# Performance work log

Hardware: AMD Instinct MI355X
Metric: run time of the kernel (lower is better)

Reference implementation:

```python
import jax, jax.numpy as jnp
import numpy as np

DIM = 768
HID = 3072
HID2 = HID // 2
MAX_LEVEL = 8
N_LEV = MAX_LEVEL + 1
BATCH, SEQ = 2, 2048
EPS = 1e-5


def _layernorm(x, gamma, beta):
    m = jnp.mean(x, axis=-1, keepdims=True)
    v = jnp.mean(jnp.square(x - m), axis=-1, keepdims=True)
    return (x - m) * jax.lax.rsqrt(v + EPS) * gamma + beta


def setup_inputs() -> dict:
    key = jax.random.key(0)
    ks = jax.random.split(key, 12)
    s = 0.02
    return {
        "x": jax.random.normal(ks[0], (BATCH, SEQ, DIM), dtype=jnp.float32),
        "levels_info": jax.random.randint(ks[1], (SEQ, 4), 0, N_LEV, dtype=jnp.int32),
        "gamma": jnp.ones((DIM,), dtype=jnp.float32),
        "beta": jnp.zeros((DIM,), dtype=jnp.float32),
        "W1": jax.random.normal(ks[2], (DIM, HID), dtype=jnp.float32) * s,
        "b1": jnp.zeros((HID,), dtype=jnp.float32),
        "W2": jax.random.normal(ks[3], (HID, DIM), dtype=jnp.float32) * s,
        "b2": jnp.zeros((DIM,), dtype=jnp.float32),
        "A1": jax.random.normal(ks[4], (N_LEV, DIM, HID2), dtype=jnp.float32) * s,
        "a1b": jnp.zeros((N_LEV, HID2), dtype=jnp.float32),
        "A2": jax.random.normal(ks[5], (N_LEV, HID2, DIM), dtype=jnp.float32) * s,
        "a2b": jnp.zeros((N_LEV, DIM), dtype=jnp.float32),
        "lmw": jnp.ones((N_LEV,), dtype=jnp.float32)
        + jax.random.normal(ks[6], (N_LEV,), dtype=jnp.float32) * 0.1,
    }


def reference(x, levels_info, gamma, beta, W1, b1, W2, b2, A1, a1b, A2, a2b, lmw):
    # x: [B,S,D]
    x_norm = _layernorm(x, gamma, beta)
    # main MLP: Linear -> GELU (exact, torch default) -> Linear; dropout=0 is identity
    h = jax.nn.gelu(jnp.einsum("bsd,dh->bsh", x_norm, W1) + b1, approximate=False)
    main_out = jnp.einsum("bsh,hd->bsd", h, W2) + b2

    # per-token depth-indexed adapter routing
    depths = jnp.clip(levels_info[:, 0], 0, MAX_LEVEL)  # [S]
    level_adapted = jnp.zeros_like(main_out)
    for lvl in range(N_LEV):  # small fixed expert set
        mask = (depths == lvl).astype(x.dtype)[None, :, None]  # [1,S,1]
        hl = jax.nn.relu(jnp.einsum("bsd,dh->bsh", x_norm, A1[lvl]) + a1b[lvl])
        level_adapted = level_adapted + mask * (
            jnp.einsum("bsh,hd->bsd", hl, A2[lvl]) + a2b[lvl]
        )

    # softmax over the sequence axis (faithful to F.softmax(..., dim=0))
    mix = jax.nn.softmax(lmw[depths], axis=0)[None, :, None]  # [1,S,1]
    return main_out * (1.0 - mix) + level_adapted * mix
```

## Files before the change

kernel.cpp:

```cpp
#include <hip/hip_runtime.h>
#include <hip/hip_bf16.h>
#include <math.h>

typedef __bf16 bf16;
typedef __bf16 bf16x4 __attribute__((ext_vector_type(4)));
typedef __bf16 bf16x8 __attribute__((ext_vector_type(8)));
typedef float f32x4 __attribute__((ext_vector_type(4)));

#define DIM 768
#define HID 3072
#define HID2 1536
#define NLEV 9
#define SEQ 2048
#define ROWS 4096
#define MAXPAD 5248
#define MAXTILES 41

__device__ __forceinline__ void gld16(const void* g, void* l) {
    __builtin_amdgcn_global_load_lds(
        (const __attribute__((address_space(1))) void*)g,
        (__attribute__((address_space(3))) void*)l, 16, 0, 0);
}

__device__ __forceinline__ float fast_gelu(float v) {
    float v2 = v * v;
    float twou = v * (1.59576912f + 0.071354816f * v2);
    float t = __expf(twou);
    return v * t / (t + 1.0f);
}


__device__ __forceinline__ void ln_body(int row, float* sm,
                                        const float* __restrict__ x,
                                        const float* __restrict__ gamma,
                                        const float* __restrict__ beta,
                                        bf16* __restrict__ xn) {
    int tid = threadIdx.x;
    const float* xr = x + (size_t)row * DIM;
    float v0 = xr[tid], v1 = xr[tid + 256], v2 = xr[tid + 512];
    float s = v0 + v1 + v2;
    float q = v0 * v0 + v1 * v1 + v2 * v2;
    for (int off = 32; off; off >>= 1) {
        s += __shfl_down(s, off, 64);
        q += __shfl_down(q, off, 64);
    }
    int wv = tid >> 6, ln = tid & 63;
    if (ln == 0) { sm[wv] = s; sm[4 + wv] = q; }
    __syncthreads();
    if (tid == 0) {
        float S = sm[0] + sm[1] + sm[2] + sm[3];
        float Q = sm[4] + sm[5] + sm[6] + sm[7];
        float m = S * (1.0f / DIM);
        float var = Q * (1.0f / DIM) - m * m;
        sm[8] = m;
        sm[9] = rsqrtf(var + 1e-5f);
    }
    __syncthreads();
    float m = sm[8], r = sm[9];
    bf16* xo = xn + (size_t)row * DIM;
    xo[tid]       = (bf16)((v0 - m) * r * gamma[tid]       + beta[tid]);
    xo[tid + 256] = (bf16)((v1 - m) * r * gamma[tid + 256] + beta[tid + 256]);
    xo[tid + 512] = (bf16)((v2 - m) * r * gamma[tid + 512] + beta[tid + 512]);
}

__device__ __forceinline__ void transpose_body64(float* sm,
                                                 const float* __restrict__ inb,
                                                 bf16* __restrict__ outb,
                                                 int R, int C, int bx, int by) {
    int tid = threadIdx.x;
    int ty = tid >> 4;
    int tx4 = (tid & 15) * 4;
#pragma unroll
    for (int p = 0; p < 4; p++) {
        int rloc = p * 16 + ty;
        int row = by * 64 + rloc;
        float4 v = *(const float4*)(inb + (size_t)row * C + bx * 64 + tx4);
        sm[rloc * 65 + tx4 + 0] = v.x;
        sm[rloc * 65 + tx4 + 1] = v.y;
        sm[rloc * 65 + tx4 + 2] = v.z;
        sm[rloc * 65 + tx4 + 3] = v.w;
    }
    __syncthreads();
    int ch = tid & 7;
    int ocb = tid >> 3;
#pragma unroll
    for (int p = 0; p < 2; p++) {
        int oc = p * 32 + ocb;
        bf16x8 tmp;
#pragma unroll
        for (int k = 0; k < 8; k++) tmp[k] = (bf16)sm[(ch * 8 + k) * 65 + oc];
        *(bf16x8*)(outb + (size_t)(bx * 64 + oc) * R + by * 64 + ch * 8) = tmp;
    }
}

__device__ __forceinline__ void routing_body(float* sm,
                                             const int* __restrict__ levels_info,
                                             const float* __restrict__ lmw,
                                             float* __restrict__ mix,
                                             int* __restrict__ row_index,
                                             int* __restrict__ tile_meta,
                                             float* __restrict__ zbuf) {
    int* cnt = (int*)sm;
    int* cur = cnt + NLEV;
    int* off = cur + NLEV;
    float* mixv = (float*)(off + NLEV);
    int tid = threadIdx.x;
    if (tid < NLEV) { cnt[tid] = 0; cur[tid] = 0; }
    __syncthreads();
    for (int s = tid; s < SEQ; s += 256) {
        int d = levels_info[s * 4];
        d = d < 0 ? 0 : (d > 8 ? 8 : d);
        atomicAdd(&cnt[d], 1);
    }
    for (int i = tid; i < MAXPAD; i += 256) row_index[i] = -1;
    for (int i = tid; i < 512; i += 256) zbuf[i] = 0.0f;
    __syncthreads();
    if (tid == 0) {
        float mx = lmw[0];
        for (int l = 1; l < NLEV; l++) mx = fmaxf(mx, lmw[l]);
        float denom = 0.f;
        for (int l = 0; l < NLEV; l++) denom += (float)cnt[l] * expf(lmw[l] - mx);
        float inv = 1.0f / denom;
        int running = 0, t = 0;
        for (int l = 0; l < NLEV; l++) {
            mixv[l] = expf(lmw[l] - mx) * inv;
            off[l] = running;
            int seg = (2 * cnt[l] + 127) & ~127;
            for (int k = 0; k < seg / 128; k++) tile_meta[t++] = l;
            running += seg;
        }
        for (; t < MAXTILES; t++) tile_meta[t] = -1;
    }
    __syncthreads();
    for (int s = tid; s < SEQ; s += 256) {
        int d = levels_info[s * 4];
        d = d < 0 ? 0 : (d > 8 ? 8 : d);
        int p = atomicAdd(&cur[d], 2);
        row_index[off[d] + p]     = s;
        row_index[off[d] + p + 1] = s + SEQ;
        mix[s] = mixv[d];
    }
}

__global__ __launch_bounds__(256) void prep_kernel(const float* __restrict__ x,
                                                   const int* __restrict__ levels_info,
                                                   const float* __restrict__ gamma,
                                                   const float* __restrict__ beta,
                                                   const float* __restrict__ W1,
                                                   const float* __restrict__ A1,
                                                   const float* __restrict__ lmw,
                                                   bf16* __restrict__ Xn,
                                                   bf16* __restrict__ W1t,
                                                   bf16* __restrict__ A1t,
                                                   float* __restrict__ mix,
                                                   int* __restrict__ row_index,
                                                   int* __restrict__ tile_meta,
                                                   float* __restrict__ zbuf) {
    __shared__ __align__(16) float sm[64 * 65];
    int bid = blockIdx.x;
    if (bid == 0) { routing_body(sm, levels_info, lmw, mix, row_index, tile_meta, zbuf); return; }
    bid -= 1;
    if (bid < ROWS) { ln_body(bid, sm, x, gamma, beta, Xn); return; }
    bid -= ROWS;
    if (bid < 576) {
        transpose_body64(sm, W1, W1t, DIM, HID, bid % 48, bid / 48);
        return;
    }
    bid -= 576;
    {
        int bz = bid / 288, r = bid % 288;
        transpose_body64(sm, A1 + (size_t)bz * DIM * HID2, A1t + (size_t)bz * DIM * HID2,
                         DIM, HID2, r % 24, r / 24);
    }
}

template<int KT>
__device__ __forceinline__ void gemm_loop_db(const bf16* ga0, const bf16* ga1,
                                             const bf16* gb0, const bf16* gb1,
                                             bf16* As, bf16* Bs,
                                             f32x4 (&acc)[4][4]) {
    int tid = threadIdx.x;
    int wv = tid >> 6;
    int lane = tid & 63;
    int wm = wv >> 1, wn = wv & 1;
    int swz = (lane >> 1) & 3;
    int achunk = ((lane >> 4) ^ swz) * 8;
    int aoff = ((wm * 64) + (lane & 15)) * 32 + achunk;
    int boff = ((wn * 64) + (lane & 15)) * 32 + achunk;
    gld16(ga0, As + wv * 512);
    gld16(ga1, As + 2048 + wv * 512);
    gld16(gb0, Bs + wv * 512);
    gld16(gb1, Bs + 2048 + wv * 512);
    ga0 += 32; ga1 += 32; gb0 += 32; gb1 += 32;
#pragma unroll
    for (int kt = 0; kt < KT; ++kt) {
        __syncthreads();
        const int cur = (kt & 1) << 12;
        const int nxt = cur ^ 4096;
        if (kt + 1 < KT) {
            gld16(ga0, As + nxt + wv * 512);
            gld16(ga1, As + nxt + 2048 + wv * 512);
            gld16(gb0, Bs + nxt + wv * 512);
            gld16(gb1, Bs + nxt + 2048 + wv * 512);
            ga0 += 32; ga1 += 32; gb0 += 32; gb1 += 32;
        }
        bf16x8 af[4], bfr[4];
#pragma unroll
        for (int i = 0; i < 4; i++) af[i] = *(const bf16x8*)(As + cur + aoff + i * 512);
#pragma unroll
        for (int j = 0; j < 4; j++) bfr[j] = *(const bf16x8*)(Bs + cur + boff + j * 512);
#pragma unroll
        for (int i = 0; i < 4; i++)
#pragma unroll
            for (int j = 0; j < 4; j++)
                acc[i][j] = __builtin_amdgcn_mfma_f32_16x16x32_bf16(af[i], bfr[j], acc[i][j], 0, 0, 0);
    }
}

#define ACC_INIT(acc) \
    _Pragma("unroll") for (int i = 0; i < 4; i++) \
    _Pragma("unroll") for (int j = 0; j < 4; j++) acc[i][j] = (f32x4){0.f, 0.f, 0.f, 0.f};

#define SWZ_CG(tid) (((tid) & 3) ^ (((tid) >> 3) & 3))

__device__ __forceinline__ void store_tile(const bf16* cbuf, int lane,
                                           bf16* gptr, int ldg) {
#pragma unroll
    for (int p = 0; p < 8; p++) {
        int lrow = p * 8 + (lane >> 3);
        int chunk = (lane & 7) * 8;
        bf16x8 v = *(const bf16x8*)(cbuf + lrow * 64 + chunk);
        *(bf16x8*)(gptr + (size_t)lrow * ldg + chunk) = v;
    }
}

__global__ __launch_bounds__(256) void mlp1_kernel(const bf16* __restrict__ Xn,
                                                   const bf16* __restrict__ W1t,
                                                   const float* __restrict__ b1,
                                                   bf16* __restrict__ H,
                                                   const bf16* __restrict__ A1t,
                                                   const float* __restrict__ a1b,
                                                   const int* __restrict__ row_index,
                                                   const int* __restrict__ tile_meta,
                                                   const bf16* __restrict__ zbuf,
                                                   bf16* __restrict__ HL,
                                                   const float* __restrict__ W2,
                                                   const float* __restrict__ A2,
                                                   bf16* __restrict__ W2t,
                                                   bf16* __restrict__ A2t) {
    __shared__ __align__(16) bf16 smem[16384];
    bf16* As = smem;
    bf16* Bs = smem + 8192;
    int bid = blockIdx.x, tid = threadIdx.x;
    int r0 = tid >> 2, cg = SWZ_CG(tid);
    int lane = tid & 63, wv = tid >> 6, wm = wv >> 1, wn = wv & 1;
    bf16* cbuf = smem + wv * 4096;

    if (bid < 768) {
        int nb = bid / 32, mb = bid % 32;
        f32x4 acc[4][4];
        ACC_INIT(acc);
        const bf16* ga0 = Xn + (size_t)(mb * 128 + r0) * DIM + cg * 8;
        const bf16* ga1 = ga0 + (size_t)64 * DIM;
        const bf16* gb0 = W1t + (size_t)(nb * 128 + r0) * DIM + cg * 8;
        const bf16* gb1 = gb0 + (size_t)64 * DIM;
        gemm_loop_db<24>(ga0, ga1, gb0, gb1, As, Bs, acc);
        int cbase = nb * 128 + wn * 64 + (lane & 15);
        __syncthreads();
#pragma unroll
        for (int j = 0; j < 4; j++) {
            float bias = b1[cbase + j * 16];
#pragma unroll
            for (int i = 0; i < 4; i++)
#pragma unroll
                for (int r = 0; r < 4; r++) {
                    int lrow = i * 16 + ((lane >> 4) << 2) + r;
                    int lcol = j * 16 + (lane & 15);
                    cbuf[lrow * 64 + lcol] = (bf16)fast_gelu(acc[i][j][r] + bias);
                }
        }
        __syncthreads();
        store_tile(cbuf, lane, H + (size_t)(mb * 128 + wm * 64) * HID + nb * 128 + wn * 64, HID);
    } else if (bid < 1260) {
        int t2 = bid - 768;
        int nb = t2 % 12, t = t2 / 12;
        int lvl = tile_meta[t];
        if (lvl < 0) return;
        f32x4 acc[4][4];
        ACC_INIT(acc);
        int ridx0 = row_index[t * 128 + r0];
        int ridx1 = row_index[t * 128 + 64 + r0];
        const bf16* ga0 = (ridx0 >= 0) ? (Xn + (size_t)ridx0 * DIM + cg * 8) : (zbuf + cg * 8);
        const bf16* ga1 = (ridx1 >= 0) ? (Xn + (size_t)ridx1 * DIM + cg * 8) : (zbuf + cg * 8);
        const bf16* Bl = A1t + (size_t)lvl * HID2 * DIM;
        const bf16* gb0 = Bl + (size_t)(nb * 128 + r0) * DIM + cg * 8;
        const bf16* gb1 = gb0 + (size_t)64 * DIM;
        gemm_loop_db<24>(ga0, ga1, gb0, gb1, As, Bs, acc);
        int cbase = nb * 128 + wn * 64 + (lane & 15);
        __syncthreads();
#pragma unroll
        for (int j = 0; j < 4; j++) {
            float bias = a1b[lvl * HID2 + cbase + j * 16];
#pragma unroll
            for (int i = 0; i < 4; i++)
#pragma unroll
                for (int r = 0; r < 4; r++) {
                    int lrow = i * 16 + ((lane >> 4) << 2) + r;
                    int lcol = j * 16 + (lane & 15);
                    cbuf[lrow * 64 + lcol] = (bf16)fmaxf(acc[i][j][r] + bias, 0.0f);
                }
        }
        __syncthreads();
        store_tile(cbuf, lane, HL + (size_t)(t * 128 + wm * 64) * HID2 + nb * 128 + wn * 64, HID2);
    } else if (bid < 1836) {
        int idx = bid - 1260;
        transpose_body64((float*)smem, W2, W2t, HID, DIM, idx % 12, idx / 12);
    } else {
        int idx = bid - 1836;
        int bz = idx / 288, r = idx % 288;
        transpose_body64((float*)smem, A2 + (size_t)bz * HID2 * DIM,
                         A2t + (size_t)bz * HID2 * DIM, HID2, DIM, r % 12, r / 12);
    }
}

__global__ __launch_bounds__(256) void mlp2_kernel(const bf16* __restrict__ H,
                                                   const bf16* __restrict__ W2t,
                                                   bf16* __restrict__ part,
                                                   const bf16* __restrict__ HL,
                                                   const bf16* __restrict__ A2t,
                                                   const float* __restrict__ a2b,
                                                   const int* __restrict__ row_index,
                                                   const int* __restrict__ tile_meta,
                                                   bf16* __restrict__ apart) {
    __shared__ __align__(16) bf16 smem[16384];
    bf16* As = smem;
    bf16* Bs = smem + 8192;
    int bid = blockIdx.x, tid = threadIdx.x;
    int r0 = tid >> 2, cg = SWZ_CG(tid);
    int lane = tid & 63, wv = tid >> 6, wm = wv >> 1, wn = wv & 1;
    bf16* cbuf = smem + wv * 4096;
    f32x4 acc[4][4];
    ACC_INIT(acc);

    if (bid < 384) {
        int cc = bid % 12;
        int nb = cc >> 1, ks = cc & 1;
        int mb = bid / 12;
        const bf16* ga0 = H + (size_t)(mb * 128 + r0) * HID + ks * 1536 + cg * 8;
        const bf16* ga1 = ga0 + (size_t)64 * HID;
        const bf16* gb0 = W2t + (size_t)(nb * 128 + r0) * HID + ks * 1536 + cg * 8;
        const bf16* gb1 = gb0 + (size_t)64 * HID;
        gemm_loop_db<48>(ga0, ga1, gb0, gb1, As, Bs, acc);
        __syncthreads();
#pragma unroll
        for (int j = 0; j < 4; j++)
#pragma unroll
            for (int i = 0; i < 4; i++)
#pragma unroll
                for (int r = 0; r < 4; r++) {
                    int lrow = i * 16 + ((lane >> 4) << 2) + r;
                    int lcol = j * 16 + (lane & 15);
                    cbuf[lrow * 64 + lcol] = (bf16)acc[i][j][r];
                }
        __syncthreads();
        bf16* pk = part + (size_t)ks * ROWS * DIM;
        store_tile(cbuf, lane, pk + (size_t)(mb * 128 + wm * 64) * DIM + nb * 128 + wn * 64, DIM);
    } else {
        int t2 = bid - 384;
        int nb = t2 % 6, t = t2 / 6;
        int lvl = tile_meta[t];
        if (lvl < 0) return;
        const bf16* ga0 = HL + (size_t)(t * 128 + r0) * HID2 + cg * 8;
        const bf16* ga1 = ga0 + (size_t)64 * HID2;
        const bf16* Bl = A2t + (size_t)lvl * DIM * HID2;
        const bf16* gb0 = Bl + (size_t)(nb * 128 + r0) * HID2 + cg * 8;
        const bf16* gb1 = gb0 + (size_t)64 * HID2;
        gemm_loop_db<48>(ga0, ga1, gb0, gb1, As, Bs, acc);
        int cbase = nb * 128 + wn * 64 + (lane & 15);
        __syncthreads();
#pragma unroll
        for (int j = 0; j < 4; j++) {
            float bias = a2b[lvl * DIM + cbase + j * 16];
#pragma unroll
            for (int i = 0; i < 4; i++)
#pragma unroll
                for (int r = 0; r < 4; r++) {
                    int lrow = i * 16 + ((lane >> 4) << 2) + r;
                    int lcol = j * 16 + (lane & 15);
                    cbuf[lrow * 64 + lcol] = (bf16)(acc[i][j][r] + bias);
                }
        }
        __syncthreads();
        int colg = nb * 128 + wn * 64;
#pragma unroll
        for (int p = 0; p < 8; p++) {
            int lrow = p * 8 + (lane >> 3);
            int chunk = (lane & 7) * 8;
            int rg = row_index[t * 128 + wm * 64 + lrow];
            if (rg >= 0) {
                bf16x8 v = *(const bf16x8*)(cbuf + lrow * 64 + chunk);
                *(bf16x8*)(apart + (size_t)rg * DIM + colg + chunk) = v;
            }
        }
    }
}

__global__ __launch_bounds__(256) void combine_kernel(const bf16* __restrict__ part,
                                                      const bf16* __restrict__ apart,
                                                      const float* __restrict__ b2,
                                                      const float* __restrict__ mix,
                                                      float* __restrict__ out) {
    int i = blockIdx.x * 256 + threadIdx.x;
    int base = i * 4;
    int row = base / DIM;
    int c = base - row * DIM;
    float mx = mix[row & (SEQ - 1)];
    bf16x4 p0 = *(const bf16x4*)(part + base);
    bf16x4 p1 = *(const bf16x4*)(part + (size_t)ROWS * DIM + base);
    bf16x4 a0 = *(const bf16x4*)(apart + base);
    float4 o;
    float* po = &o.x;
#pragma unroll
    for (int k = 0; k < 4; k++) {
        float main_v = (float)p0[k] + (float)p1[k] + b2[c + k];
        po[k] = (1.0f - mx) * main_v + mx * (float)a0[k];
    }
    *(float4*)(out + base) = o;
}

extern "C" void kernel_launch(void* const* d_in, const int* in_sizes, int n_in,
                              void* d_out, int out_size, void* d_ws, size_t ws_size,
                              hipStream_t stream) {
    const float* x    = (const float*)d_in[0];
    const int* levels = (const int*)d_in[1];
    const float* gamma= (const float*)d_in[2];
    const float* beta = (const float*)d_in[3];
    const float* W1   = (const float*)d_in[4];
    const float* b1   = (const float*)d_in[5];
    const float* W2   = (const float*)d_in[6];
    const float* b2   = (const float*)d_in[7];
    const float* A1   = (const float*)d_in[8];
    const float* a1b  = (const float*)d_in[9];
    const float* A2   = (const float*)d_in[10];
    const float* a2b  = (const float*)d_in[11];
    const float* lmw  = (const float*)d_in[12];
    float* out = (float*)d_out;

    char* p = (char*)d_ws;
    auto alloc = [&](size_t bytes) {
        char* r = p;
        p += (bytes + 255) & ~(size_t)255;
        return r;
    };
    bf16* Xn   = (bf16*)alloc((size_t)ROWS * DIM * 2);
    bf16* W1t  = (bf16*)alloc((size_t)HID * DIM * 2);
    bf16* W2t  = (bf16*)alloc((size_t)DIM * HID * 2);
    bf16* A1t  = (bf16*)alloc((size_t)NLEV * HID2 * DIM * 2);
    bf16* A2t  = (bf16*)alloc((size_t)NLEV * DIM * HID2 * 2);
    bf16* H    = (bf16*)alloc((size_t)ROWS * HID * 2);
    bf16* HL   = (bf16*)alloc((size_t)MAXPAD * HID2 * 2);
    bf16* part = (bf16*)alloc((size_t)2 * ROWS * DIM * 2);
    bf16* apart= (bf16*)alloc((size_t)ROWS * DIM * 2);
    float* mix = (float*)alloc(SEQ * 4);
    int* row_index = (int*)alloc(MAXPAD * 4);
    int* tile_meta = (int*)alloc(MAXTILES * 4);
    float* zbuf    = (float*)alloc(2048);

    prep_kernel<<<dim3(1 + ROWS + 576 + 2592), dim3(256), 0, stream>>>(
        x, levels, gamma, beta, W1, A1, lmw,
        Xn, W1t, A1t, mix, row_index, tile_meta, zbuf);

    mlp1_kernel<<<dim3(768 + 492 + 576 + 2592), dim3(256), 0, stream>>>(
        Xn, W1t, b1, H, A1t, a1b, row_index, tile_meta, (const bf16*)zbuf, HL,
        W2, A2, W2t, A2t);

    mlp2_kernel<<<dim3(384 + MAXTILES * 6), dim3(256), 0, stream>>>(
        H, W2t, part, HL, A2t, a2b, row_index, tile_meta, apart);

    combine_kernel<<<dim3(ROWS * DIM / 1024), dim3(256), 0, stream>>>(
        part, apart, b2, mix, out);
}
```

Baseline: 285.4 us.

## Use one wave per LayerNorm row and interleave prep and GEMM block schedules

LayerNorm now gives each 64-lane wave its own row, four rows per block, with float4 loads and a shuffle-xor reduction, so the shared-memory barriers go away and the LN grid shrinks fourfold. The prep kernel interleaves LN blocks with weight-transpose blocks, and the mlp1 kernel interleaves the leading blocks of its two segments: the 1260 blocks below index 1260 alternate with the next 1260. Both remappings aim to mix different work types across CUs and balance load. The block-index mapping is more complex, and the LN variance still uses the E[x²]-m² form.

```diff
diff --git a/kernel.cpp b/kernel.cpp
--- a/kernel.cpp
+++ b/kernel.cpp
@@ -30,37 +30,46 @@
 }
 
 
-__device__ __forceinline__ void ln_body(int row, float* sm,
-                                        const float* __restrict__ x,
-                                        const float* __restrict__ gamma,
-                                        const float* __restrict__ beta,
-                                        bf16* __restrict__ xn) {
+__device__ __forceinline__ void ln4_body(int blk,
+                                         const float* __restrict__ x,
+                                         const float* __restrict__ gamma,
+                                         const float* __restrict__ beta,
+                                         bf16* __restrict__ xn) {
     int tid = threadIdx.x;
+    int wv = tid >> 6, ln = tid & 63;
+    int row = blk * 4 + wv;
     const float* xr = x + (size_t)row * DIM;
-    float v0 = xr[tid], v1 = xr[tid + 256], v2 = xr[tid + 512];
-    float s = v0 + v1 + v2;
-    float q = v0 * v0 + v1 * v1 + v2 * v2;
+    int c = ln * 4;
+    float4 v0 = *(const float4*)(xr + c);
+    float4 v1 = *(const float4*)(xr + c + 256);
+    float4 v2 = *(const float4*)(xr + c + 512);
+    float s = v0.x + v0.y + v0.z + v0.w
+            + v1.x + v1.y + v1.z + v1.w
+            + v2.x + v2.y + v2.z + v2.w;
+    float q = v0.x * v0.x + v0.y * v0.y + v0.z * v0.z + v0.w * v0.w
+            + v1.x * v1.x + v1.y * v1.y + v1.z * v1.z + v1.w * v1.w
+            + v2.x * v2.x + v2.y * v2.y + v2.z * v2.z + v2.w * v2.w;
+#pragma unroll
     for (int off = 32; off; off >>= 1) {
-        s += __shfl_down(s, off, 64);
-        q += __shfl_down(q, off, 64);
-    }
-    int wv = tid >> 6, ln = tid & 63;
-    if (ln == 0) { sm[wv] = s; sm[4 + wv] = q; }
-    __syncthreads();
-    if (tid == 0) {
-        float S = sm[0] + sm[1] + sm[2] + sm[3];
-        float Q = sm[4] + sm[5] + sm[6] + sm[7];
-        float m = S * (1.0f / DIM);
-        float var = Q * (1.0f / DIM) - m * m;
-        sm[8] = m;
-        sm[9] = rsqrtf(var + 1e-5f);
-    }
-    __syncthreads();
-    float m = sm[8], r = sm[9];
+        s += __shfl_xor(s, off, 64);
+        q += __shfl_xor(q, off, 64);
+    }
+    float m = s * (1.0f / DIM);
+    float r = rsqrtf(q * (1.0f / DIM) - m * m + 1e-5f);
     bf16* xo = xn + (size_t)row * DIM;
-    xo[tid]       = (bf16)((v0 - m) * r * gamma[tid]       + beta[tid]);
-    xo[tid + 256] = (bf16)((v1 - m) * r * gamma[tid + 256] + beta[tid + 256]);
-    xo[tid + 512] = (bf16)((v2 - m) * r * gamma[tid + 512] + beta[tid + 512]);
+#pragma unroll
+    for (int p = 0; p < 3; p++) {
+        int cc = c + p * 256;
+        float4 v = (p == 0) ? v0 : (p == 1) ? v1 : v2;
+        float4 g = *(const float4*)(gamma + cc);
+        float4 b = *(const float4*)(beta + cc);
+        bf16x4 o;
+        o[0] = (bf16)((v.x - m) * r * g.x + b.x);
+        o[1] = (bf16)((v.y - m) * r * g.y + b.y);
+        o[2] = (bf16)((v.z - m) * r * g.z + b.z);
+        o[3] = (bf16)((v.w - m) * r * g.w + b.w);
+        *(bf16x4*)(xo + cc) = o;
+    }
 }
 
 __device__ __forceinline__ void transpose_body64(float* sm,
@@ -157,18 +166,23 @@
                                                    int* __restrict__ tile_meta,
                                                    float* __restrict__ zbuf) {
     __shared__ __align__(16) float sm[64 * 65];
-    int bid = blockIdx.x;
-    if (bid == 0) { routing_body(sm, levels_info, lmw, mix, row_index, tile_meta, zbuf); return; }
-    bid -= 1;
-    if (bid < ROWS) { ln_body(bid, sm, x, gamma, beta, Xn); return; }
-    bid -= ROWS;
-    if (bid < 576) {
-        transpose_body64(sm, W1, W1t, DIM, HID, bid % 48, bid / 48);
+    int b = blockIdx.x;
+    if (b == 0) { routing_body(sm, levels_info, lmw, mix, row_index, tile_meta, zbuf); return; }
+    int i = b - 1;
+    int tb;
+    if (i < 4096) {
+        if ((i & 3) == 0) { ln4_body(i >> 2, x, gamma, beta, Xn); return; }
+        tb = (i >> 2) * 3 + (i & 3) - 1;
+    } else {
+        tb = 3072 + (i - 4096);
+    }
+    if (tb < 576) {
+        transpose_body64(sm, W1, W1t, DIM, HID, tb % 48, tb / 48);
         return;
     }
-    bid -= 576;
+    tb -= 576;
     {
-        int bz = bid / 288, r = bid % 288;
+        int bz = tb / 288, r = tb % 288;
         transpose_body64(sm, A1 + (size_t)bz * DIM * HID2, A1t + (size_t)bz * DIM * HID2,
                          DIM, HID2, r % 24, r / 24);
     }
@@ -251,7 +265,9 @@
     __shared__ __align__(16) bf16 smem[16384];
     bf16* As = smem;
     bf16* Bs = smem + 8192;
-    int bid = blockIdx.x, tid = threadIdx.x;
+    int b = blockIdx.x;
+    int bid = (b < 2520) ? ((b & 1) ? (1260 + (b >> 1)) : (b >> 1)) : b;
+    int tid = threadIdx.x;
     int r0 = tid >> 2, cg = SWZ_CG(tid);
     int lane = tid & 63, wv = tid >> 6, wm = wv >> 1, wn = wv & 1;
     bf16* cbuf = smem + wv * 4096;
@@ -466,7 +482,7 @@
     int* tile_meta = (int*)alloc(MAXTILES * 4);
     float* zbuf    = (float*)alloc(2048);
 
-    prep_kernel<<<dim3(1 + ROWS + 576 + 2592), dim3(256), 0, stream>>>(
+    prep_kernel<<<dim3(1 + 1024 + 576 + 2592), dim3(256), 0, stream>>>(
         x, levels, gamma, beta, W1, A1, lmw,
         Xn, W1t, A1t, mix, row_index, tile_meta, zbuf);
 
```

Result: slower. 309.6 us (+8.5%).
